# Kernel optimization log

Measured on AMD Instinct MI355X. Metric: run time of the kernel, lower is better.

Reference implementation:

```python
import jax, jax.numpy as jnp
import numpy as np


def phi(x):
    # ELU + 1 feature map (Katharopoulos et al. 2020)
    return jax.nn.elu(x) + 1.0


def setup_inputs() -> dict:
    key = jax.random.key(0)
    k1, k2, k3 = jax.random.split(key, 3)
    B, T, D = 2, 2048, 512
    x = jax.random.normal(k1, (B, T, D), dtype=jnp.float32)
    # torch nn.Linear stores weight as (out_features, in_features)
    w_qkv = jax.random.normal(k2, (3 * D, D), dtype=jnp.float32) * 0.02
    w_out = jax.random.normal(k3, (D, D), dtype=jnp.float32) * 0.02
    return {"x": x, "w_qkv": w_qkv, "w_out": w_out, "n_heads": 16}


def reference(x, w_qkv, w_out, n_heads):
    B, T, D = x.shape
    H = n_heads
    Dh = D // H
    qkv = x @ w_qkv.T                                   # (B,T,3D)
    qkv = qkv.reshape(B, T, 3, H, Dh).transpose(2, 0, 3, 1, 4)  # (3,B,H,T,Dh)
    q, k, v = phi(qkv[0]), phi(qkv[1]), qkv[2]
    # kv outer product: (B,H,T,Dh_k,Dh_v), causal cumsum over time
    kv = k[..., :, None] * v[..., None, :]
    kv_cumsum = jnp.cumsum(kv, axis=2)
    num = jnp.einsum('bhtd,bhtde->bhte', q, kv_cumsum)  # (B,H,T,Dh)
    k_cumsum = jnp.cumsum(k, axis=2)
    denom = jnp.einsum('bhtd,bhtd->bht', q, k_cumsum)[..., None]
    denom = jnp.maximum(denom, 1e-6)
    out = num / denom                                   # (B,H,T,Dh)
    out = out.transpose(0, 2, 1, 3).reshape(B, T, D)
    return out @ w_out.T
```

## Files before the change

### kernel.cpp

```cpp
#include <hip/hip_runtime.h>
#include <hip/hip_bf16.h>
#include <math.h>

#define B_ 2
#define T_ 2048
#define D_ 512
#define H_ 16
#define DH 32
#define L_ 64
#define C_ 32
#define NC 1024
#define VTP 72

typedef __attribute__((ext_vector_type(8))) short bf16x8;
typedef __attribute__((ext_vector_type(4))) float f32x4;
typedef __attribute__((ext_vector_type(4))) unsigned short u16x4;

#define AS1 __attribute__((address_space(1)))
#define AS3 __attribute__((address_space(3)))

__device__ __forceinline__ float bf2f(unsigned short u) {
    union { float f; unsigned int i; } v; v.i = ((unsigned int)u) << 16; return v.f;
}
__device__ __forceinline__ unsigned short f2bf(float f) {
    union { float f; unsigned int u; } v; v.f = f;
    unsigned int u = v.u;
    unsigned int r = u + 0x7FFFu + ((u >> 16) & 1u);
    return (unsigned short)(r >> 16);
}
__device__ __forceinline__ unsigned short f2bf_rne(float f) {
    __hip_bfloat16 h = __float2bfloat16(f);
    union { __hip_bfloat16 h; unsigned short u; } v; v.h = h; return v.u;
}
__device__ __forceinline__ bf16x8 phi_frag(bf16x8 in) {
    bf16x8 r;
    #pragma unroll
    for (int i = 0; i < 8; ++i) {
        float f = bf2f((unsigned short)in[i]);
        f = f > 0.f ? f + 1.f : __expf(f);
        r[i] = (short)f2bf(f);
    }
    return r;
}
__device__ __forceinline__ void gload_lds16(const unsigned short* g, unsigned short* l) {
    __builtin_amdgcn_global_load_lds((const AS1 unsigned int*)g, (AS3 unsigned int*)l, 16, 0, 0);
}

template<int BM, bool AF32, bool OUT_BF16>
__global__ __launch_bounds__(256) void gemm_nt(const void* __restrict__ Aptr,
                                               const float* __restrict__ Wf,
                                               void* __restrict__ Cout,
                                               int N, int K)
{
    constexpr int MF = BM / 32;
    constexpr int AF4 = BM / 32;
    __shared__ unsigned short As[2][BM][32];
    __shared__ unsigned short Bs[2][128][32];
    const int tid = threadIdx.x;
    const int lane = tid & 63;
    const int wave = tid >> 6;
    const int wr = wave >> 1;
    const int wc = wave & 1;
    const size_t bm = (size_t)blockIdx.x * BM;
    const size_t bn = (size_t)blockIdx.y * 128;

    const int r8 = lane >> 3;
    const int c4 = (lane & 7) * 4;
    const int lrow = lane >> 2;
    const int lcol = (lane & 3) * 8;

    const float* agf = nullptr;
    const unsigned short* agb = nullptr;
    if constexpr (AF32) agf = (const float*)Aptr + (bm + wave * (BM / 4) + r8) * (size_t)K + c4;
    else                agb = (const unsigned short*)Aptr + (bm + wave * (BM / 4) + lrow) * (size_t)K + lcol;
    const float* wgf = Wf + (bn + wave * 32 + r8) * (size_t)K + c4;

    f32x4 aL[AF4];
    f32x4 wL[4];

    auto load_stage = [&](int buf, int k0) {
        if constexpr (AF32) {
            #pragma unroll
            for (int i = 0; i < AF4; ++i)
                aL[i] = *(const f32x4*)(agf + k0 + (size_t)(i * 8) * K);
        } else {
            gload_lds16(agb + k0, &As[buf][wave * (BM / 4)][0]);
            if constexpr (BM / 4 == 32)
                gload_lds16(agb + (size_t)16 * K + k0, &As[buf][wave * (BM / 4) + 16][0]);
        }
        #pragma unroll
        for (int i = 0; i < 4; ++i)
            wL[i] = *(const f32x4*)(wgf + k0 + (size_t)(i * 8) * K);
    };
    auto write_stage = [&](int buf) {
        if constexpr (AF32) {
            #pragma unroll
            for (int i = 0; i < AF4; ++i) {
                u16x4 o;
                o.x = f2bf_rne(aL[i][0]); o.y = f2bf_rne(aL[i][1]);
                o.z = f2bf_rne(aL[i][2]); o.w = f2bf_rne(aL[i][3]);
                *(u16x4*)&As[buf][wave * (BM / 4) + r8 + i * 8][c4] = o;
            }
        }
        #pragma unroll
        for (int i = 0; i < 4; ++i) {
            u16x4 o;
            o.x = f2bf_rne(wL[i][0]); o.y = f2bf_rne(wL[i][1]);
            o.z = f2bf_rne(wL[i][2]); o.w = f2bf_rne(wL[i][3]);
            *(u16x4*)&Bs[buf][wave * 32 + r8 + i * 8][c4] = o;
        }
    };

    f32x4 acc[MF][4];
    #pragma unroll
    for (int m = 0; m < MF; ++m)
        #pragma unroll
        for (int n = 0; n < 4; ++n)
            acc[m][n] = (f32x4){0.f, 0.f, 0.f, 0.f};

    const int rr = lane & 15;
    const int kb = (lane >> 4) * 8;

    load_stage(0, 0);
    write_stage(0);
    __syncthreads();
    int cur = 0;
    for (int k0 = 0; k0 < K; k0 += 32) {
        const bool more = k0 + 32 < K;
        if (more) load_stage(cur ^ 1, k0 + 32);
        bf16x8 af[MF], bfr[4];
        #pragma unroll
        for (int m = 0; m < MF; ++m)
            af[m] = *(const bf16x8*)&As[cur][wr * (BM / 2) + m * 16 + rr][kb];
        #pragma unroll
        for (int n = 0; n < 4; ++n)
            bfr[n] = *(const bf16x8*)&Bs[cur][wc * 64 + n * 16 + rr][kb];
        #pragma unroll
        for (int m = 0; m < MF; ++m)
            #pragma unroll
            for (int n = 0; n < 4; ++n)
                acc[m][n] = __builtin_amdgcn_mfma_f32_16x16x32_bf16(af[m], bfr[n], acc[m][n], 0, 0, 0);
        if (more) write_stage(cur ^ 1);
        __syncthreads();
        cur ^= 1;
    }

    const int cr = (lane >> 4) * 4;
    const int cc = lane & 15;
    #pragma unroll
    for (int m = 0; m < MF; ++m)
        #pragma unroll
        for (int n = 0; n < 4; ++n)
            #pragma unroll
            for (int j = 0; j < 4; ++j) {
                size_t row = bm + wr * (BM / 2) + m * 16 + cr + j;
                size_t col = bn + wc * 64 + n * 16 + cc;
                float v = acc[m][n][j];
                if (OUT_BF16) ((unsigned short*)Cout)[row * N + col] = f2bf(v);
                else          ((float*)Cout)[row * N + col] = v;
            }
}

__global__ __launch_bounds__(256) void chunk_sum(const unsigned short* __restrict__ qkv,
                                                 float* __restrict__ cSf)
{
    __shared__ unsigned short Kt[4][DH][VTP];
    __shared__ unsigned short Vt[4][48][VTP];
    const int tid = threadIdx.x;
    const int lane = tid & 63;
    const int wave = tid >> 6;
    const int chunk = blockIdx.x * 4 + wave;
    const int c = chunk & 31;
    const int h = (chunk >> 5) & 15;
    const int b = chunk >> 9;
    const size_t rowbase = ((size_t)(b * T_ + c * L_)) * (3 * D_) + h * DH;
    const int half = lane & 1;

    #pragma unroll
    for (int it = 0; it < 2; ++it) {
        int t = (lane >> 1) + it * 32;
        const unsigned short* kp = qkv + rowbase + (size_t)t * (3 * D_) + D_ + half * 16;
        const unsigned short* vp = qkv + rowbase + (size_t)t * (3 * D_) + 2 * D_ + half * 16;
        bf16x8 k0 = phi_frag(*(const bf16x8*)kp);
        bf16x8 k1 = phi_frag(*(const bf16x8*)(kp + 8));
        bf16x8 v0 = *(const bf16x8*)vp;
        bf16x8 v1 = *(const bf16x8*)(vp + 8);
        #pragma unroll
        for (int i = 0; i < 8; ++i) {
            Kt[wave][half * 16 + i][t]     = (unsigned short)k0[i];
            Kt[wave][half * 16 + 8 + i][t] = (unsigned short)k1[i];
            Vt[wave][half * 16 + i][t]     = (unsigned short)v0[i];
            Vt[wave][half * 16 + 8 + i][t] = (unsigned short)v1[i];
        }
    }
    Vt[wave][32][lane] = 0x3F80;

    const int fr = lane & 15;
    const int fg = lane >> 4;
    f32x4 acc[3][2];
    #pragma unroll
    for (int m = 0; m < 3; ++m)
        #pragma unroll
        for (int n = 0; n < 2; ++n)
            acc[m][n] = (f32x4){0.f, 0.f, 0.f, 0.f};

    #pragma unroll
    for (int ks = 0; ks < 2; ++ks) {
        int toff = fg * 8 + ks * 32;
        bf16x8 av[3], bk[2];
        #pragma unroll
        for (int m = 0; m < 3; ++m) av[m] = *(const bf16x8*)&Vt[wave][m * 16 + fr][toff];
        #pragma unroll
        for (int n = 0; n < 2; ++n) bk[n] = *(const bf16x8*)&Kt[wave][n * 16 + fr][toff];
        #pragma unroll
        for (int m = 0; m < 3; ++m)
            #pragma unroll
            for (int n = 0; n < 2; ++n)
                acc[m][n] = __builtin_amdgcn_mfma_f32_16x16x32_bf16(av[m], bk[n], acc[m][n], 0, 0, 0);
    }

    float* outp = cSf + (size_t)chunk * (48 * 32);
    #pragma unroll
    for (int m = 0; m < 2; ++m)
        #pragma unroll
        for (int n = 0; n < 2; ++n)
            #pragma unroll
            for (int r = 0; r < 4; ++r)
                outp[(m * 16 + fg * 4 + r) * 32 + n * 16 + fr] = acc[m][n][r];
    if (fg == 0) {
        #pragma unroll
        for (int n = 0; n < 2; ++n)
            outp[32 * 32 + n * 16 + fr] = acc[2][n][0];
    }
}

__global__ __launch_bounds__(256) void chunk_scan(const float* __restrict__ cSf,
                                                  unsigned short* __restrict__ cSt)
{
    int idx = blockIdx.x * 256 + threadIdx.x;
    int bh = idx / (33 * 32);
    int r  = idx % (33 * 32);
    const float* src = cSf + (size_t)bh * C_ * (48 * 32) + r;
    unsigned short* dst = cSt + (size_t)bh * C_ * (48 * 32) + r;
    float v[C_];
    #pragma unroll
    for (int c = 0; c < C_; ++c) v[c] = src[(size_t)c * (48 * 32)];
    float acc = 0.f;
    #pragma unroll
    for (int c = 0; c < C_; ++c) {
        dst[(size_t)c * (48 * 32)] = f2bf(acc);
        acc += v[c];
    }
}

__global__ __launch_bounds__(256) void chunk_out(const unsigned short* __restrict__ qkv,
                                                 const unsigned short* __restrict__ cSt,
                                                 unsigned short* __restrict__ attn)
{
    __shared__ unsigned short Vt[2][48][VTP];
    __shared__ unsigned short Am[4][32][VTP];
    const int tid = threadIdx.x;
    const int lane = tid & 63;
    const int wave = tid >> 6;
    const int ci = wave >> 1;
    const int wh = wave & 1;
    const int chunk = blockIdx.x * 2 + ci;
    const int c = chunk & 31;
    const int h = (chunk >> 5) & 15;
    const int b = chunk >> 9;
    const size_t rowbase = ((size_t)(b * T_ + c * L_)) * (3 * D_) + h * DH;
    const int fr = lane & 15;
    const int fg = lane >> 4;

    {
        int t = wh * 32 + (lane >> 1);
        int half = lane & 1;
        const unsigned short* vp = qkv + rowbase + (size_t)t * (3 * D_) + 2 * D_ + half * 16;
        bf16x8 v0 = *(const bf16x8*)vp;
        bf16x8 v1 = *(const bf16x8*)(vp + 8);
        #pragma unroll
        for (int i = 0; i < 8; ++i) {
            Vt[ci][half * 16 + i][t]     = (unsigned short)v0[i];
            Vt[ci][half * 16 + 8 + i][t] = (unsigned short)v1[i];
        }
        if (half == 0) Vt[ci][32][t] = 0x3F80;
    }

    bf16x8 aq[2];
    #pragma unroll
    for (int mm = 0; mm < 2; ++mm) {
        int m = wh * 2 + mm;
        const unsigned short* qp = qkv + rowbase + (size_t)(m * 16 + fr) * (3 * D_) + fg * 8;
        aq[mm] = phi_frag(*(const bf16x8*)qp);
    }
    bf16x8 bk[4];
    const int nmax = wh * 2 + 1;
    #pragma unroll
    for (int n = 0; n < 4; ++n) {
        if (n <= nmax) {
            const unsigned short* kp = qkv + rowbase + (size_t)(n * 16 + fr) * (3 * D_) + D_ + fg * 8;
            bk[n] = phi_frag(*(const bf16x8*)kp);
        }
    }
    bf16x8 bkv[3];
    #pragma unroll
    for (int n = 0; n < 3; ++n)
        bkv[n] = *(const bf16x8*)&cSt[(size_t)chunk * 1536 + (size_t)(n * 16 + fr) * 32 + fg * 8];

    f32x4 zero = (f32x4){0.f, 0.f, 0.f, 0.f};
    f32x4 acc[2][3];
    #pragma unroll
    for (int mm = 0; mm < 2; ++mm)
        #pragma unroll
        for (int n = 0; n < 3; ++n)
            acc[mm][n] = __builtin_amdgcn_mfma_f32_16x16x32_bf16(aq[mm], bkv[n], zero, 0, 0, 0);

    #pragma unroll
    for (int mm = 0; mm < 2; ++mm) {
        int m = wh * 2 + mm;
        #pragma unroll
        for (int n = 0; n < 4; ++n) {
            if (n <= m) {
                f32x4 s = __builtin_amdgcn_mfma_f32_16x16x32_bf16(aq[mm], bk[n], zero, 0, 0, 0);
                #pragma unroll
                for (int r = 0; r < 4; ++r) {
                    unsigned short v = f2bf(s[r]);
                    if (n == m && fr > fg * 4 + r) v = 0;
                    Am[wave][mm * 16 + fg * 4 + r][n * 16 + fr] = v;
                }
            }
        }
    }
    {
        int zc = wh ? 48 : 16;
        *(uint2*)&Am[wave][fr][zc + fg * 4] = (uint2){0u, 0u};
    }
    __syncthreads();

    #pragma unroll
    for (int ks = 0; ks < 2; ++ks) {
        if (ks <= wh) {
            bf16x8 bv[3];
            #pragma unroll
            for (int n = 0; n < 3; ++n)
                bv[n] = *(const bf16x8*)&Vt[ci][n * 16 + fr][fg * 8 + ks * 32];
            #pragma unroll
            for (int mm = 0; mm < 2; ++mm) {
                bf16x8 aa = *(const bf16x8*)&Am[wave][mm * 16 + fr][fg * 8 + ks * 32];
                #pragma unroll
                for (int n = 0; n < 3; ++n)
                    acc[mm][n] = __builtin_amdgcn_mfma_f32_16x16x32_bf16(aa, bv[n], acc[mm][n], 0, 0, 0);
            }
        }
    }

    #pragma unroll
    for (int mm = 0; mm < 2; ++mm) {
        float dn[4];
        #pragma unroll
        for (int r = 0; r < 4; ++r)
            dn[r] = __shfl(acc[mm][2][r], lane & 48);
        #pragma unroll
        for (int r = 0; r < 4; ++r) {
            float inv = 1.0f / fmaxf(dn[r], 1e-6f);
            #pragma unroll
            for (int n = 0; n < 2; ++n)
                Am[wave][mm * 16 + fg * 4 + r][n * 16 + fr] = f2bf(acc[mm][n][r] * inv);
        }
    }
    {
        int lrow = lane >> 1;
        int half = lane & 1;
        uint4 q0 = *(const uint4*)&Am[wave][lrow][half * 16];
        uint4 q1 = *(const uint4*)&Am[wave][lrow][half * 16 + 8];
        size_t grow = (size_t)(b * T_ + c * L_ + wh * 32 + lrow);
        unsigned short* dst = attn + grow * D_ + h * DH + half * 16;
        *(uint4*)dst = q0;
        *(uint4*)(dst + 8) = q1;
    }
}

extern "C" void kernel_launch(void* const* d_in, const int* in_sizes, int n_in,
                              void* d_out, int out_size, void* d_ws, size_t ws_size,
                              hipStream_t stream) {
    const float* x     = (const float*)d_in[0];
    const float* w_qkv = (const float*)d_in[1];
    const float* w_out = (const float*)d_in[2];
    float* out = (float*)d_out;

    char* ws = (char*)d_ws;
    unsigned short* qkvb  = (unsigned short*)ws;
    unsigned short* attnb = (unsigned short*)(ws + 12582912);
    float* cSf            = (float*)(ws + 16777216);
    unsigned short* cSt   = (unsigned short*)(ws + 23068672);

    gemm_nt<128, true, true><<<dim3(4096 / 128, 1536 / 128), 256, 0, stream>>>(
        x, w_qkv, qkvb, 1536, 512);

    chunk_sum<<<NC / 4, 256, 0, stream>>>(qkvb, cSf);

    chunk_scan<<<132, 256, 0, stream>>>(cSf, cSt);

    chunk_out<<<NC / 2, 256, 0, stream>>>(qkvb, cSt, attnb);

    gemm_nt<64, false, false><<<dim3(4096 / 64, 512 / 128), 256, 0, stream>>>(
        attnb, w_out, out, 512, 512);
}
```

Baseline: 48.84 us.

## Fuse chunk prefix scan into chunk_out by redundant per-block prefix summation

Removes the separate chunk_scan kernel and has each chunk_out block recompute the exclusive prefix sum of chunk states by summing all preceding chunk states from global memory, staging them in shared memory and converting to bf16 for the MFMA. The chunk-state stride is compacted from 1536 to 1056 floats. This saves one kernel launch and the bf16 intermediate round trip, at the cost of redundant O(C^2) global reads (up to 31 chunk states per block) and an extra __syncthreads.

```diff
diff --git a/kernel.cpp b/kernel.cpp
--- a/kernel.cpp
+++ b/kernel.cpp
@@ -11,6 +11,8 @@
 #define C_ 32
 #define NC 1024
 #define VTP 72
+#define CSZ 1056
+#define PST 36
 
 typedef __attribute__((ext_vector_type(8))) short bf16x8;
 typedef __attribute__((ext_vector_type(4))) float f32x4;
@@ -219,7 +221,7 @@
                 acc[m][n] = __builtin_amdgcn_mfma_f32_16x16x32_bf16(av[m], bk[n], acc[m][n], 0, 0, 0);
     }
 
-    float* outp = cSf + (size_t)chunk * (48 * 32);
+    float* outp = cSf + (size_t)chunk * CSZ;
     #pragma unroll
     for (int m = 0; m < 2; ++m)
         #pragma unroll
@@ -234,31 +236,13 @@
     }
 }
 
-__global__ __launch_bounds__(256) void chunk_scan(const float* __restrict__ cSf,
-                                                  unsigned short* __restrict__ cSt)
-{
-    int idx = blockIdx.x * 256 + threadIdx.x;
-    int bh = idx / (33 * 32);
-    int r  = idx % (33 * 32);
-    const float* src = cSf + (size_t)bh * C_ * (48 * 32) + r;
-    unsigned short* dst = cSt + (size_t)bh * C_ * (48 * 32) + r;
-    float v[C_];
-    #pragma unroll
-    for (int c = 0; c < C_; ++c) v[c] = src[(size_t)c * (48 * 32)];
-    float acc = 0.f;
-    #pragma unroll
-    for (int c = 0; c < C_; ++c) {
-        dst[(size_t)c * (48 * 32)] = f2bf(acc);
-        acc += v[c];
-    }
-}
-
 __global__ __launch_bounds__(256) void chunk_out(const unsigned short* __restrict__ qkv,
-                                                 const unsigned short* __restrict__ cSt,
+                                                 const float* __restrict__ cSf,
                                                  unsigned short* __restrict__ attn)
 {
     __shared__ unsigned short Vt[2][48][VTP];
     __shared__ unsigned short Am[4][32][VTP];
+    __shared__ float P[2][48 * PST];
     const int tid = threadIdx.x;
     const int lane = tid & 63;
     const int wave = tid >> 6;
@@ -285,7 +269,6 @@
         }
         if (half == 0) Vt[ci][32][t] = 0x3F80;
     }
-
     bf16x8 aq[2];
     #pragma unroll
     for (int mm = 0; mm < 2; ++mm) {
@@ -302,10 +285,48 @@
             bk[n] = phi_frag(*(const bf16x8*)kp);
         }
     }
+
+    for (int idx = tid; idx < 2 * 15 * PST; idx += 256) {
+        int pi = idx / (15 * PST);
+        P[pi][33 * PST + idx % (15 * PST)] = 0.f;
+    }
+    {
+        const int c1 = (blockIdx.x * 2) & 31;
+        const int cbase = blockIdx.x * 2 - c1;
+        float s[5] = {0.f, 0.f, 0.f, 0.f, 0.f};
+        #pragma unroll 4
+        for (int j = 0; j < c1; ++j) {
+            const float* sp = cSf + (size_t)(cbase + j) * CSZ;
+            #pragma unroll
+            for (int u = 0; u < 5; ++u) {
+                int e = tid + u * 256;
+                if (e < CSZ) s[u] += sp[e];
+            }
+        }
+        const float* sc = cSf + (size_t)(blockIdx.x * 2) * CSZ;
+        #pragma unroll
+        for (int u = 0; u < 5; ++u) {
+            int e = tid + u * 256;
+            if (e < CSZ) {
+                int r_ = e >> 5, c_ = e & 31;
+                P[0][r_ * PST + c_] = s[u];
+                P[1][r_ * PST + c_] = s[u] + sc[e];
+            }
+        }
+    }
+    __syncthreads();
+
     bf16x8 bkv[3];
     #pragma unroll
-    for (int n = 0; n < 3; ++n)
-        bkv[n] = *(const bf16x8*)&cSt[(size_t)chunk * 1536 + (size_t)(n * 16 + fr) * 32 + fg * 8];
+    for (int n = 0; n < 3; ++n) {
+        f32x4 lo = *(const f32x4*)&P[ci][(n * 16 + fr) * PST + fg * 8];
+        f32x4 hi = *(const f32x4*)&P[ci][(n * 16 + fr) * PST + fg * 8 + 4];
+        #pragma unroll
+        for (int i = 0; i < 4; ++i) {
+            bkv[n][i]     = (short)f2bf(lo[i]);
+            bkv[n][4 + i] = (short)f2bf(hi[i]);
+        }
+    }
 
     f32x4 zero = (f32x4){0.f, 0.f, 0.f, 0.f};
     f32x4 acc[2][3];
@@ -392,16 +413,13 @@
     unsigned short* qkvb  = (unsigned short*)ws;
     unsigned short* attnb = (unsigned short*)(ws + 12582912);
     float* cSf            = (float*)(ws + 16777216);
-    unsigned short* cSt   = (unsigned short*)(ws + 23068672);
 
     gemm_nt<128, true, true><<<dim3(4096 / 128, 1536 / 128), 256, 0, stream>>>(
         x, w_qkv, qkvb, 1536, 512);
 
     chunk_sum<<<NC / 4, 256, 0, stream>>>(qkvb, cSf);
 
-    chunk_scan<<<132, 256, 0, stream>>>(cSf, cSt);
-
-    chunk_out<<<NC / 2, 256, 0, stream>>>(qkvb, cSt, attnb);
+    chunk_out<<<NC / 2, 256, 0, stream>>>(qkvb, cSf, attnb);
 
     gemm_nt<64, false, false><<<dim3(4096 / 64, 512 / 128), 256, 0, stream>>>(
         attnb, w_out, out, 512, 512);
```

New measurement: 84.47 us. 73.0% more time.
